# Kernel tuning notes

Measured on AMD Instinct MI355X. Metric: run time of the kernel, lower is better.

The kernel has to match this reference:

```python
import jax, jax.numpy as jnp
import numpy as np
import math

V, TB, C, H, L = 50257, 1024, 1024, 16, 8
B, T = 2, 1024
D = C // H


def setup_inputs() -> dict:
    key = jax.random.key(0)
    ks = jax.random.split(key, 16)
    s = 0.02
    n = lambda k, shp: (jax.random.normal(k, shp, jnp.float32) * s)
    inp = {
        "idx": jax.random.randint(ks[0], (B, T), 0, V),
        "tok_emb": n(ks[1], (V, C)),
        "pos_emb": n(ks[2], (1, TB, C)),
        # per-layer stacked params (torch Linear convention: W is [out, in])
        "Wq": n(ks[3], (L, C, C)), "bq": jnp.zeros((L, C)),
        "Wk": n(ks[4], (L, C, C)), "bk": jnp.zeros((L, C)),
        "Wv": n(ks[5], (L, C, C)), "bv": jnp.zeros((L, C)),
        "Wp": n(ks[6], (L, C, C)), "bp": jnp.zeros((L, C)),
        "ln1_w": jnp.ones((L, C)), "ln1_b": jnp.zeros((L, C)),
        "ln2_w": jnp.ones((L, C)), "ln2_b": jnp.zeros((L, C)),
        "W1": n(ks[7], (L, 4 * C, C)), "b1": jnp.zeros((L, 4 * C)),
        "W2": n(ks[8], (L, C, 4 * C)), "b2": jnp.zeros((L, C)),
        "lnf_w": jnp.ones((C,)), "lnf_b": jnp.zeros((C,)),
        "head_w": n(ks[9], (V, C)),
    }
    return inp


def _layer_norm(x, w, b, eps=1e-5):
    mu = x.mean(-1, keepdims=True)
    var = x.var(-1, keepdims=True)
    return (x - mu) * jax.lax.rsqrt(var + eps) * w + b


def _gpt_forward(idx, tok_emb, pos_emb, Wq, bq, Wk, bk, Wv, bv, Wp, bp,
                 ln1_w, ln1_b, ln2_w, ln2_b, W1, b1, W2, b2, lnf_w, lnf_b, head_w):
    b, t = idx.shape
    x = tok_emb[idx] + pos_emb[:, :t, :]  # [B, T, C]; drop = identity (eval)
    causal = jnp.tril(jnp.ones((t, t), dtype=bool))  # [T, T]
    scale = 1.0 / math.sqrt(D)

    def block(x, p):
        (wq, bq_, wk, bk_, wv, bv_, wp, bp_, l1w, l1b, l2w, l2b, w1, b1_, w2, b2_) = p
        h = _layer_norm(x, l1w, l1b)
        q = (h @ wq.T + bq_).reshape(b, t, H, D).transpose(0, 2, 1, 3)  # [B,H,T,D]
        k = (h @ wk.T + bk_).reshape(b, t, H, D).transpose(0, 2, 1, 3)
        v = (h @ wv.T + bv_).reshape(b, t, H, D).transpose(0, 2, 1, 3)
        att = jnp.einsum("bhqd,bhkd->bhqk", q, k) * scale
        att = jnp.where(causal, att, -jnp.inf)
        att = jax.nn.softmax(att, axis=-1)
        y = jnp.einsum("bhqk,bhkd->bhqd", att, v)
        y = y.transpose(0, 2, 1, 3).reshape(b, t, C)
        x = x + (y @ wp.T + bp_)
        h2 = _layer_norm(x, l2w, l2b)
        m = jax.nn.gelu(h2 @ w1.T + b1_, approximate=False)  # torch nn.GELU (erf)
        x = x + (m @ w2.T + b2_)
        return x, None

    params = (Wq, bq, Wk, bk, Wv, bv, Wp, bp, ln1_w, ln1_b, ln2_w, ln2_b, W1, b1, W2, b2)
    x, _ = jax.lax.scan(block, x, params)
    x = _layer_norm(x, lnf_w, lnf_b)
    logits = x @ head_w.T  # [B, T, V]
    return logits


def reference(idx, tok_emb, pos_emb, Wq, bq, Wk, bk, Wv, bv, Wp, bp,
              ln1_w, ln1_b, ln2_w, ln2_b, W1, b1, W2, b2, lnf_w, lnf_b, head_w):
    return _gpt_forward(idx, tok_emb, pos_emb, Wq, bq, Wk, bk, Wv, bv, Wp, bp,
                        ln1_w, ln1_b, ln2_w, ln2_b, W1, b1, W2, b2, lnf_w, lnf_b, head_w)
```

## Files before the change

### kernel.cpp

```cpp
#include <hip/hip_runtime.h>
#include <math.h>

#define V_ 50257
#define C_ 1024
#define H_ 16
#define L_ 8
#define B_ 2
#define T_ 1024
#define BT_ 2048
#define CC_ (C_*C_)
#define QLD_ 3072

typedef unsigned short ushort_t;
using bf16x8 = __attribute__((ext_vector_type(8))) short;
using f32x4  = __attribute__((ext_vector_type(4))) float;

#define AS1 __attribute__((address_space(1)))
#define AS3 __attribute__((address_space(3)))
#define VMCNT0() asm volatile("s_waitcnt vmcnt(0)" ::: "memory")

__device__ __forceinline__ ushort_t f2bf(float f){
  union { float f; unsigned u; } a; a.f = f;
  unsigned r = a.u + 0x7fffu + ((a.u >> 16) & 1u);
  return (ushort_t)(r >> 16);
}

__device__ __forceinline__ float wave_sum(float v){
  #pragma unroll
  for(int o=32;o>0;o>>=1) v += __shfl_down(v,o,64);
  return v;
}

__global__ __launch_bounds__(256) void cvt_blk(const float* __restrict__ s, ushort_t* __restrict__ d,
    long inner4, int nblk, long dstStride4){
  long total = inner4 * nblk;
  for(long i = (long)blockIdx.x*256 + threadIdx.x; i < total; i += (long)gridDim.x*256){
    long blk = i / inner4, r = i - blk*inner4;
    float4 v = ((const float4*)s)[i];
    ushort4 o; o.x=f2bf(v.x); o.y=f2bf(v.y); o.z=f2bf(v.z); o.w=f2bf(v.w);
    ((ushort4*)d)[blk*dstStride4 + r] = o;
  }
}

__global__ __launch_bounds__(256) void pack_qkv_bias(const float* __restrict__ bq,
    const float* __restrict__ bk, const float* __restrict__ bv, float* __restrict__ dst){
  int i = blockIdx.x*256 + threadIdx.x;
  int l = i / QLD_, c = i - l*QLD_;
  float v;
  if(c < C_)            v = bq[l*C_ + c];
  else if(c < 2*C_)     v = bk[l*C_ + c - C_];
  else                  v = bv[l*C_ + c - 2*C_];
  dst[i] = v;
}

__global__ __launch_bounds__(256) void embed_kernel(const int* __restrict__ idx,
    const float* __restrict__ tok, const float* __restrict__ pos, float* __restrict__ x){
  int i = blockIdx.x*256 + threadIdx.x;
  int c = i & (C_-1); int bt = i >> 10; int t = bt & (T_-1);
  x[i] = tok[(size_t)idx[bt]*C_ + c] + pos[t*C_ + c];
}

__global__ __launch_bounds__(256) void ln_kernel(const float* in, const float* __restrict__ w,
    const float* __restrict__ b, float* outF, ushort_t* outB){
  int row = blockIdx.x;
  const float* xr = in + (size_t)row*C_;
  float vals[4]; float sum=0.f, sq=0.f;
  #pragma unroll
  for(int l=0;l<4;l++){ float v = xr[threadIdx.x + l*256]; vals[l]=v; sum+=v; sq+=v*v; }
  __shared__ float r1[4], r2[4];
  float s1 = wave_sum(sum), s2 = wave_sum(sq);
  int wid = threadIdx.x>>6, lane = threadIdx.x&63;
  if(lane==0){ r1[wid]=s1; r2[wid]=s2; }
  __syncthreads();
  float tot  = r1[0]+r1[1]+r1[2]+r1[3];
  float tot2 = r2[0]+r2[1]+r2[2]+r2[3];
  float mu  = tot * (1.f/C_);
  float var = tot2 * (1.f/C_) - mu*mu;
  float inv = rsqrtf(var + 1e-5f);
  #pragma unroll
  for(int l=0;l<4;l++){
    int c = threadIdx.x + l*256;
    float v = (vals[l]-mu)*inv*w[c] + b[c];
    if(outB) outB[(size_t)row*C_ + c] = f2bf(v);
    else     outF[(size_t)row*C_ + c] = v;
  }
}

template<int BN>
__global__ __launch_bounds__(256) void gemm_mfma(
    const ushort_t* __restrict__ A, const ushort_t* __restrict__ W,
    const float* __restrict__ bias, const float* resid,
    float* outF, ushort_t* outB,
    int M, int N, int K, int act, int nt)
{
  constexpr int BM = 128;
  constexpr int NSB = BN/16;
  constexpr int NBF = BN/32;
  __shared__ __align__(16) short sA[2][8*512];
  __shared__ __align__(16) short sB[2][NSB*512];
  const int tid  = threadIdx.x;
  const int lane = tid & 63, wid = tid >> 6;
  const int wr = wid >> 1, wc = wid & 1;
  const int nwg = gridDim.x * gridDim.y;
  const int lid = blockIdx.x + gridDim.x * blockIdx.y;
  const int swz = (lid & 7) * (nwg >> 3) + (lid >> 3);
  const int m0 = (swz % gridDim.x) * BM, n0 = (swz / gridDim.x) * BN;
  const int r16 = lane & 15, kq = lane >> 4;

  auto stage = [&](int buf, int k0){
    #pragma unroll
    for(int s2=0; s2<2; ++s2){
      int s = wid*2 + s2;
      const ushort_t* g = A + (size_t)(m0 + s*16 + r16)*K + k0 + kq*8;
      __builtin_amdgcn_global_load_lds((const AS1 void*)g,
          (AS3 void*)&sA[buf][s*512], 16, 0, 0);
    }
    #pragma unroll
    for(int s2=0; s2<NSB/4; ++s2){
      int s = wid*(NSB/4) + s2;
      int gn = n0 + s*16 + r16; if(gn >= N) gn = N-1;
      const ushort_t* g = W + (size_t)gn*K + k0 + kq*8;
      __builtin_amdgcn_global_load_lds((const AS1 void*)g,
          (AS3 void*)&sB[buf][s*512], 16, 0, 0);
    }
  };

  f32x4 acc[4][NBF];
  #pragma unroll
  for(int i=0;i<4;i++)
    #pragma unroll
    for(int j=0;j<NBF;j++) acc[i][j] = (f32x4){0.f,0.f,0.f,0.f};

  const int NT = K >> 5;
  stage(0, 0);
  int cur = 0;
  for(int t=0; t<NT; ++t){
    __syncthreads();
    if(t+1 < NT) stage(cur^1, (t+1)*32);
    bf16x8 af[4], bfr[NBF];
    #pragma unroll
    for(int m=0;m<4;m++) af[m] = *(const bf16x8*)&sA[cur][(wr*4+m)*512 + lane*8];
    #pragma unroll
    for(int n=0;n<NBF;n++) bfr[n] = *(const bf16x8*)&sB[cur][(wc*NBF+n)*512 + lane*8];
    #pragma unroll
    for(int m=0;m<4;m++)
      #pragma unroll
      for(int n=0;n<NBF;n++)
        acc[m][n] = __builtin_amdgcn_mfma_f32_16x16x32_bf16(af[m], bfr[n], acc[m][n], 0, 0, 0);
    cur ^= 1;
  }

  const int colb = n0 + wc*(BN/2);
  #pragma unroll
  for(int m=0;m<4;m++){
    int rowb = m0 + wr*64 + m*16 + kq*4;
    #pragma unroll
    for(int n=0;n<NBF;n++){
      int col = colb + n*16 + r16;
      if(col >= N) continue;
      float bv = bias ? bias[col] : 0.f;
      #pragma unroll
      for(int i=0;i<4;i++){
        int row = rowb + i;
        float v = acc[m][n][i] + bv;
        if(act) v = 0.5f*v*(1.f + erff(v*0.70710678118654752f));
        if(resid) v += resid[(size_t)row*N + col];
        if(outB) outB[(size_t)row*N + col] = f2bf(v);
        else if(nt) __builtin_nontemporal_store(v, &outF[(size_t)row*N + col]);
        else outF[(size_t)row*N + col] = v;
      }
    }
  }
}

__global__ __launch_bounds__(256) void flash_kernel(const ushort_t* __restrict__ qkv,
    ushort_t* __restrict__ y){
  const int tid = threadIdx.x, lane = tid & 63, wid = tid >> 6;
  const int r16 = lane & 15, kq = lane >> 4;
  const int lid = blockIdx.x + 16*blockIdx.y;
  const int swz = (lid & 7)*64 + (lid >> 3);
  const int qt = swz & 15, bh = swz >> 4;
  const int b = bh >> 4, h = bh & 15;
  const int q0 = qt*64, qw0 = q0 + wid*16;
  const int qa = qw0 + r16;

  __shared__ __align__(16) short Kt[2][8][512];
  __shared__ __align__(16) short VT[2][64][68];
  __shared__ __align__(16) short Pl[4][16][68];
  __shared__ __align__(16) short Ol[4][16][68];

  const size_t rowQ = (size_t)(b*T_ + qa)*QLD_ + h*64 + kq*8;
  bf16x8 qf0 = *(const bf16x8*)(qkv + rowQ);
  bf16x8 qf1 = *(const bf16x8*)(qkv + rowQ + 32);

  auto stageK = [&](int buf, int jt){
    #pragma unroll
    for(int s2=0;s2<2;s2++){
      int s = wid*2 + s2;
      const ushort_t* g = qkv + (size_t)(b*T_ + jt*64 + (s>>1)*16 + r16)*QLD_
                          + C_ + h*64 + (s&1)*32 + kq*8;
      __builtin_amdgcn_global_load_lds((const AS1 void*)g,
          (AS3 void*)&Kt[buf][s][lane*8], 16, 0, 0);
    }
  };

  f32x4 acc[4];
  #pragma unroll
  for(int t=0;t<4;t++) acc[t] = (f32x4){0.f,0.f,0.f,0.f};
  float m_r = -INFINITY, l_r = 0.f;

  {
    stageK(0, 0);
    const ushort_t* vg = qkv + (size_t)(b*T_ + lane)*QLD_ + 2*C_ + h*64;
    bf16x8 va = *(const bf16x8*)(vg + wid*8);
    bf16x8 vb = *(const bf16x8*)(vg + 32 + wid*8);
    VMCNT0();
    #pragma unroll
    for(int j=0;j<8;j++){ VT[0][wid*8+j][lane]=va[j]; VT[0][32+wid*8+j][lane]=vb[j]; }
    __syncthreads();
  }

  const int njt = qt + 1;
  for(int jt=0; jt<njt; ++jt){
    const int cur = jt & 1;
    const bool more = (jt+1) < njt;
    bf16x8 vr0, vr1;
    if(more){
      stageK(cur^1, jt+1);
      const ushort_t* vg = qkv + (size_t)(b*T_ + (jt+1)*64 + lane)*QLD_ + 2*C_ + h*64;
      vr0 = *(const bf16x8*)(vg + wid*8);
      vr1 = *(const bf16x8*)(vg + 32 + wid*8);
    }

    f32x4 st[4];
    __builtin_amdgcn_s_setprio(1);
    #pragma unroll
    for(int kr=0;kr<4;kr++){
      st[kr] = (f32x4){0.f,0.f,0.f,0.f};
      st[kr] = __builtin_amdgcn_mfma_f32_16x16x32_bf16(*(const bf16x8*)&Kt[cur][kr*2+0][lane*8], qf0, st[kr], 0,0,0);
      st[kr] = __builtin_amdgcn_mfma_f32_16x16x32_bf16(*(const bf16x8*)&Kt[cur][kr*2+1][lane*8], qf1, st[kr], 0,0,0);
    }
    __builtin_amdgcn_s_setprio(0);

    float vals[16]; float mx = m_r;
    if(jt == njt-1){
      #pragma unroll
      for(int kr=0;kr<4;kr++)
        #pragma unroll
        for(int i=0;i<4;i++){
          int ka = jt*64 + kr*16 + 4*kq + i;
          float v = (ka <= qa) ? st[kr][i]*0.125f : -INFINITY;
          vals[kr*4+i] = v; mx = fmaxf(mx, v);
        }
    } else {
      #pragma unroll
      for(int kr=0;kr<4;kr++)
        #pragma unroll
        for(int i=0;i<4;i++){
          float v = st[kr][i]*0.125f;
          vals[kr*4+i] = v; mx = fmaxf(mx, v);
        }
    }
    mx = fmaxf(mx, __shfl_xor(mx, 16, 64));
    mx = fmaxf(mx, __shfl_xor(mx, 32, 64));
    float alpha = __expf(m_r - mx);
    float ps = 0.f;
    #pragma unroll
    for(int kr=0;kr<4;kr++){
      float p0 = __expf(vals[kr*4+0]-mx), p1 = __expf(vals[kr*4+1]-mx);
      float p2 = __expf(vals[kr*4+2]-mx), p3 = __expf(vals[kr*4+3]-mx);
      ps += (p0+p1)+(p2+p3);
      unsigned u0 = (unsigned)f2bf(p0) | ((unsigned)f2bf(p1)<<16);
      unsigned u1 = (unsigned)f2bf(p2) | ((unsigned)f2bf(p3)<<16);
      *(unsigned*)&Pl[wid][r16][kr*16 + 4*kq]     = u0;
      *(unsigned*)&Pl[wid][r16][kr*16 + 4*kq + 2] = u1;
    }
    ps += __shfl_xor(ps, 16, 64);
    ps += __shfl_xor(ps, 32, 64);
    l_r = l_r*alpha + ps; m_r = mx;
    #pragma unroll
    for(int t=0;t<4;t++)
      #pragma unroll
      for(int j=0;j<4;j++) acc[t][j] *= alpha;

    union { bf16x8 v8; uint2 u2[2]; } pf, vf;
    __builtin_amdgcn_s_setprio(1);
    #pragma unroll
    for(int ks2=0; ks2<2; ks2++){
      pf.u2[0] = *(const uint2*)&Pl[wid][r16][ks2*32 + kq*8];
      pf.u2[1] = *(const uint2*)&Pl[wid][r16][ks2*32 + kq*8 + 4];
      #pragma unroll
      for(int db=0; db<4; db++){
        vf.u2[0] = *(const uint2*)&VT[cur][16*db + r16][ks2*32 + kq*8];
        vf.u2[1] = *(const uint2*)&VT[cur][16*db + r16][ks2*32 + kq*8 + 4];
        acc[db] = __builtin_amdgcn_mfma_f32_16x16x32_bf16(vf.v8, pf.v8, acc[db], 0,0,0);
      }
    }
    __builtin_amdgcn_s_setprio(0);

    if(more){
      VMCNT0();
      #pragma unroll
      for(int j=0;j<8;j++){ VT[cur^1][wid*8+j][lane]=vr0[j]; VT[cur^1][32+wid*8+j][lane]=vr1[j]; }
    }
    __syncthreads();
  }

  float linv = 1.f / l_r;
  #pragma unroll
  for(int db=0; db<4; db++)
    #pragma unroll
    for(int i=0;i<4;i++)
      Ol[wid][r16][16*db + 4*kq + i] = (short)f2bf(acc[db][i]*linv);
  int q = lane >> 2, c0 = (lane & 3)*16;
  const short* src = &Ol[wid][q][c0];
  uint2 a0 = *(const uint2*)(src+0), a1 = *(const uint2*)(src+4);
  uint2 a2 = *(const uint2*)(src+8), a3 = *(const uint2*)(src+12);
  ushort_t* dst = y + (size_t)(b*T_ + qw0 + q)*C_ + h*64 + c0;
  uint4 w0 = {a0.x, a0.y, a1.x, a1.y}, w1 = {a2.x, a2.y, a3.x, a3.y};
  *(uint4*)(dst+0) = w0;
  *(uint4*)(dst+8) = w1;
}

__global__ __launch_bounds__(256) void gemm_nt(const float* __restrict__ A, const float* __restrict__ W,
    const float* __restrict__ bias, const float* resid, float* Cm,
    int M, int N, int K, int act){
  __shared__ float As[16][68];
  __shared__ float Bs[16][68];
  int m0 = blockIdx.y*64, n0 = blockIdx.x*64;
  int tid = threadIdx.x;
  int tx = tid & 15, ty = tid >> 4;
  float acc[4][4] = {};
  for(int k0=0;k0<K;k0+=16){
    #pragma unroll
    for(int l=0;l<4;l++){
      int li = tid + l*256;
      int r = li >> 4, c = li & 15;
      int gm = m0 + r, gn = n0 + r, gk = k0 + c;
      As[c][r] = (gm<M) ? A[(size_t)gm*K + gk] : 0.f;
      Bs[c][r] = (gn<N) ? W[(size_t)gn*K + gk] : 0.f;
    }
    __syncthreads();
    #pragma unroll
    for(int k=0;k<16;k++){
      float4 av = *(const float4*)&As[k][ty*4];
      float4 bv = *(const float4*)&Bs[k][tx*4];
      float a[4] = {av.x, av.y, av.z, av.w};
      float b4[4] = {bv.x, bv.y, bv.z, bv.w};
      #pragma unroll
      for(int i=0;i<4;i++)
        #pragma unroll
        for(int j=0;j<4;j++)
          acc[i][j] = fmaf(a[i], b4[j], acc[i][j]);
    }
    __syncthreads();
  }
  #pragma unroll
  for(int i=0;i<4;i++){
    int m = m0 + ty*4 + i; if(m>=M) continue;
    #pragma unroll
    for(int j=0;j<4;j++){
      int n = n0 + tx*4 + j; if(n>=N) continue;
      float v = acc[i][j];
      if(bias) v += bias[n];
      if(act)  v = 0.5f*v*(1.f + erff(v*0.70710678118654752f));
      if(resid) v += resid[(size_t)m*N + n];
      Cm[(size_t)m*N + n] = v;
    }
  }
}

extern "C" void kernel_launch(void* const* d_in, const int* in_sizes, int n_in,
                              void* d_out, int out_size, void* d_ws, size_t ws_size,
                              hipStream_t stream) {
  const int*   idx  = (const int*)  d_in[0];
  const float* tok  = (const float*)d_in[1];
  const float* pos  = (const float*)d_in[2];
  const float* Wq   = (const float*)d_in[3];
  const float* bq   = (const float*)d_in[4];
  const float* Wk   = (const float*)d_in[5];
  const float* bk   = (const float*)d_in[6];
  const float* Wv   = (const float*)d_in[7];
  const float* bv   = (const float*)d_in[8];
  const float* Wp   = (const float*)d_in[9];
  const float* bp   = (const float*)d_in[10];
  const float* ln1w = (const float*)d_in[11];
  const float* ln1b = (const float*)d_in[12];
  const float* ln2w = (const float*)d_in[13];
  const float* ln2b = (const float*)d_in[14];
  const float* W1   = (const float*)d_in[15];
  const float* b1   = (const float*)d_in[16];
  const float* W2   = (const float*)d_in[17];
  const float* b2   = (const float*)d_in[18];
  const float* lnfw = (const float*)d_in[19];
  const float* lnfb = (const float*)d_in[20];
  const float* headw= (const float*)d_in[21];

  float* out = (float*)d_out;
  ushort_t* qkvb = (ushort_t*)(out);
  ushort_t* hb   = (ushort_t*)(out + 3145728);
  ushort_t* yb   = (ushort_t*)(out + 4194304);
  ushort_t* mb   = (ushort_t*)(out + 5242880);
  ushort_t* wqkv = (ushort_t*)(out + 9437184);
  ushort_t* wpb  = (ushort_t*)(out + 22020096);
  ushort_t* w1b  = (ushort_t*)(out + 26214400);
  ushort_t* w2b  = (ushort_t*)(out + 42991616);
  float*    bqkv = out + 59768832;
  float*    x    = (float*)d_ws;
  ushort_t* xb   = (ushort_t*)((float*)d_ws + 2097152);
  ushort_t* whb  = (ushort_t*)((float*)d_ws + 3145728);
  const bool big = ws_size >= (size_t)28877312 * 4;

  cvt_blk<<<2048,256,0,stream>>>(Wq, wqkv,          CC_/4, L_, 3*CC_/4);
  cvt_blk<<<2048,256,0,stream>>>(Wk, wqkv + CC_,    CC_/4, L_, 3*CC_/4);
  cvt_blk<<<2048,256,0,stream>>>(Wv, wqkv + 2*CC_,  CC_/4, L_, 3*CC_/4);
  cvt_blk<<<2048,256,0,stream>>>(Wp, wpb,  (long)L_*CC_/4,   1, (long)L_*CC_/4);
  cvt_blk<<<2048,256,0,stream>>>(W1, w1b,  (long)L_*CC_,     1, (long)L_*CC_);
  cvt_blk<<<2048,256,0,stream>>>(W2, w2b,  (long)L_*CC_,     1, (long)L_*CC_);
  if(big) cvt_blk<<<2048,256,0,stream>>>(headw, whb, (long)V_*C_/4, 1, (long)V_*C_/4);
  pack_qkv_bias<<<L_*QLD_/256,256,0,stream>>>(bq, bk, bv, bqkv);

  embed_kernel<<<BT_*C_/256, 256, 0, stream>>>(idx, tok, pos, x);

  for(int l=0;l<L_;l++){
    ln_kernel<<<BT_,256,0,stream>>>(x, ln1w + l*C_, ln1b + l*C_, nullptr, hb);
    gemm_mfma<128><<<dim3(BT_/128, QLD_/128),256,0,stream>>>(hb, wqkv + (size_t)l*3*CC_,
        bqkv + l*QLD_, nullptr, nullptr, qkvb, BT_, QLD_, C_, 0, 0);
    flash_kernel<<<dim3(T_/64, B_*H_),256,0,stream>>>(qkvb, yb);
    gemm_mfma<64><<<dim3(BT_/128, C_/64),256,0,stream>>>(yb, wpb + (size_t)l*CC_,
        bp + l*C_, x, x, nullptr, BT_, C_, C_, 0, 0);
    ln_kernel<<<BT_,256,0,stream>>>(x, ln2w + l*C_, ln2b + l*C_, nullptr, hb);
    gemm_mfma<128><<<dim3(BT_/128, 4*C_/128),256,0,stream>>>(hb, w1b + (size_t)l*4*CC_,
        b1 + (size_t)l*4*C_, nullptr, nullptr, mb, BT_, 4*C_, C_, 1, 0);
    gemm_mfma<64><<<dim3(BT_/128, C_/64),256,0,stream>>>(mb, w2b + (size_t)l*4*CC_,
        b2 + l*C_, x, x, nullptr, BT_, C_, 4*C_, 0, 0);
  }

  if(big){
    ln_kernel<<<BT_,256,0,stream>>>(x, lnfw, lnfb, nullptr, xb);
    gemm_mfma<128><<<dim3(BT_/128, (V_+127)/128),256,0,stream>>>(xb, whb,
        nullptr, nullptr, out, nullptr, BT_, V_, C_, 0, 1);
  } else {
    ln_kernel<<<BT_,256,0,stream>>>(x, lnfw, lnfb, x, nullptr);
    gemm_nt<<<dim3((V_+63)/64, BT_/64),256,0,stream>>>(x, headw, nullptr, nullptr, out,
                                                       BT_, V_, C_, 0);
  }
}
```

Baseline: 2.871 ms.

## Fold softmax scale into Q projection and use lazy rescaling in flash attention

Moves the 1/sqrt(D) scale into the QKV GEMM epilogue for the Q columns, so the attention kernel no longer multiplies every score. The online softmax now rescales the accumulator and running sum only when the new block max exceeds the running max by more than a threshold (wave-wide vote). The bf16 packing of probabilities uses the hardware v_cvt_pk_bf16_f32 instruction instead of manual rounding. The lazy rescale lets exponentials exceed 1 (up to e^8), which risks precision loss, and Q is now rounded to bf16 after scaling.

```diff
diff --git a/kernel.cpp b/kernel.cpp
--- a/kernel.cpp
+++ b/kernel.cpp
@@ -23,6 +23,12 @@
   union { float f; unsigned u; } a; a.f = f;
   unsigned r = a.u + 0x7fffu + ((a.u >> 16) & 1u);
   return (ushort_t)(r >> 16);
+}
+
+__device__ __forceinline__ unsigned cvtpk_bf16(float a, float b){
+  unsigned r;
+  asm("v_cvt_pk_bf16_f32 %0, %1, %2" : "=v"(r) : "v"(a), "v"(b));
+  return r;
 }
 
 __device__ __forceinline__ float wave_sum(float v){
@@ -91,7 +97,7 @@
     const ushort_t* __restrict__ A, const ushort_t* __restrict__ W,
     const float* __restrict__ bias, const float* resid,
     float* outF, ushort_t* outB,
-    int M, int N, int K, int act, int nt)
+    int M, int N, int K, int act, int nt, int qs)
 {
   constexpr int BM = 128;
   constexpr int NSB = BN/16;
@@ -163,6 +169,7 @@
       for(int i=0;i<4;i++){
         int row = rowb + i;
         float v = acc[m][n][i] + bv;
+        if(qs && col < C_) v *= 0.125f;
         if(act) v = 0.5f*v*(1.f + erff(v*0.70710678118654752f));
         if(resid) v += resid[(size_t)row*N + col];
         if(outB) outB[(size_t)row*N + col] = f2bf(v);
@@ -242,46 +249,53 @@
     }
     __builtin_amdgcn_s_setprio(0);
 
-    float vals[16]; float mx = m_r;
+    float vals[16];
     if(jt == njt-1){
       #pragma unroll
       for(int kr=0;kr<4;kr++)
         #pragma unroll
         for(int i=0;i<4;i++){
           int ka = jt*64 + kr*16 + 4*kq + i;
-          float v = (ka <= qa) ? st[kr][i]*0.125f : -INFINITY;
-          vals[kr*4+i] = v; mx = fmaxf(mx, v);
+          vals[kr*4+i] = (ka <= qa) ? st[kr][i] : -INFINITY;
         }
     } else {
       #pragma unroll
       for(int kr=0;kr<4;kr++)
         #pragma unroll
-        for(int i=0;i<4;i++){
-          float v = st[kr][i]*0.125f;
-          vals[kr*4+i] = v; mx = fmaxf(mx, v);
-        }
-    }
-    mx = fmaxf(mx, __shfl_xor(mx, 16, 64));
-    mx = fmaxf(mx, __shfl_xor(mx, 32, 64));
-    float alpha = __expf(m_r - mx);
+        for(int i=0;i<4;i++) vals[kr*4+i] = st[kr][i];
+    }
+    float t8[8];
+    #pragma unroll
+    for(int i=0;i<8;i++) t8[i] = fmaxf(vals[i], vals[i+8]);
+    float t4a = fmaxf(t8[0],t8[4]), t4b = fmaxf(t8[1],t8[5]);
+    float t4c = fmaxf(t8[2],t8[6]), t4d = fmaxf(t8[3],t8[7]);
+    float pmax = fmaxf(fmaxf(t4a,t4b), fmaxf(t4c,t4d));
+    pmax = fmaxf(pmax, __shfl_xor(pmax, 16, 64));
+    pmax = fmaxf(pmax, __shfl_xor(pmax, 32, 64));
+
+    if(!__all(pmax - m_r <= 8.f)){
+      float mnew = fmaxf(m_r, pmax);
+      float alpha = __expf(m_r - mnew);
+      l_r *= alpha;
+      #pragma unroll
+      for(int t=0;t<4;t++)
+        #pragma unroll
+        for(int j=0;j<4;j++) acc[t][j] *= alpha;
+      m_r = mnew;
+    }
+
     float ps = 0.f;
     #pragma unroll
     for(int kr=0;kr<4;kr++){
-      float p0 = __expf(vals[kr*4+0]-mx), p1 = __expf(vals[kr*4+1]-mx);
-      float p2 = __expf(vals[kr*4+2]-mx), p3 = __expf(vals[kr*4+3]-mx);
+      float p0 = __expf(vals[kr*4+0]-m_r), p1 = __expf(vals[kr*4+1]-m_r);
+      float p2 = __expf(vals[kr*4+2]-m_r), p3 = __expf(vals[kr*4+3]-m_r);
       ps += (p0+p1)+(p2+p3);
-      unsigned u0 = (unsigned)f2bf(p0) | ((unsigned)f2bf(p1)<<16);
-      unsigned u1 = (unsigned)f2bf(p2) | ((unsigned)f2bf(p3)<<16);
-      *(unsigned*)&Pl[wid][r16][kr*16 + 4*kq]     = u0;
-      *(unsigned*)&Pl[wid][r16][kr*16 + 4*kq + 2] = u1;
+      *(unsigned*)&Pl[wid][r16][kr*16 + 4*kq]     = cvtpk_bf16(p0, p1);
+      *(unsigned*)&Pl[wid][r16][kr*16 + 4*kq + 2] = cvtpk_bf16(p2, p3);
     }
     ps += __shfl_xor(ps, 16, 64);
     ps += __shfl_xor(ps, 32, 64);
-    l_r = l_r*alpha + ps; m_r = mx;
-    #pragma unroll
-    for(int t=0;t<4;t++)
-      #pragma unroll
-      for(int j=0;j<4;j++) acc[t][j] *= alpha;
+    l_r += ps;
 
     union { bf16x8 v8; uint2 u2[2]; } pf, vf;
     __builtin_amdgcn_s_setprio(1);
@@ -425,21 +439,21 @@
   for(int l=0;l<L_;l++){
     ln_kernel<<<BT_,256,0,stream>>>(x, ln1w + l*C_, ln1b + l*C_, nullptr, hb);
     gemm_mfma<128><<<dim3(BT_/128, QLD_/128),256,0,stream>>>(hb, wqkv + (size_t)l*3*CC_,
-        bqkv + l*QLD_, nullptr, nullptr, qkvb, BT_, QLD_, C_, 0, 0);
+        bqkv + l*QLD_, nullptr, nullptr, qkvb, BT_, QLD_, C_, 0, 0, 1);
     flash_kernel<<<dim3(T_/64, B_*H_),256,0,stream>>>(qkvb, yb);
     gemm_mfma<64><<<dim3(BT_/128, C_/64),256,0,stream>>>(yb, wpb + (size_t)l*CC_,
-        bp + l*C_, x, x, nullptr, BT_, C_, C_, 0, 0);
+        bp + l*C_, x, x, nullptr, BT_, C_, C_, 0, 0, 0);
     ln_kernel<<<BT_,256,0,stream>>>(x, ln2w + l*C_, ln2b + l*C_, nullptr, hb);
     gemm_mfma<128><<<dim3(BT_/128, 4*C_/128),256,0,stream>>>(hb, w1b + (size_t)l*4*CC_,
-        b1 + (size_t)l*4*C_, nullptr, nullptr, mb, BT_, 4*C_, C_, 1, 0);
+        b1 + (size_t)l*4*C_, nullptr, nullptr, mb, BT_, 4*C_, C_, 1, 0, 0);
     gemm_mfma<64><<<dim3(BT_/128, C_/64),256,0,stream>>>(mb, w2b + (size_t)l*4*CC_,
-        b2 + l*C_, x, x, nullptr, BT_, C_, 4*C_, 0, 0);
+        b2 + l*C_, x, x, nullptr, BT_, C_, 4*C_, 0, 0, 0);
   }
 
   if(big){
     ln_kernel<<<BT_,256,0,stream>>>(x, lnfw, lnfb, nullptr, xb);
     gemm_mfma<128><<<dim3(BT_/128, (V_+127)/128),256,0,stream>>>(xb, whb,
-        nullptr, nullptr, out, nullptr, BT_, V_, C_, 0, 1);
+        nullptr, nullptr, out, nullptr, BT_, V_, C_, 0, 1, 0);
   } else {
     ln_kernel<<<BT_,256,0,stream>>>(x, lnfw, lnfb, x, nullptr);
     gemm_nt<<<dim3((V_+63)/64, BT_/64),256,0,stream>>>(x, headw, nullptr, nullptr, out,
```

Result: no change. 2.861 ms (-0.4%).
